# Kernel optimization log

Measured on AMD Instinct MI355X. Metric: run time of the kernel, lower is better.

## Reference

```python
import jax, jax.numpy as jnp
import numpy as np

B, L, D, H = 8, 2048, 1024, 16
FACTOR = 3


def setup_inputs() -> dict:
    key = jax.random.key(0)
    ks = jax.random.split(key, 11)
    s = 0.02
    mk = lambda k, shp: jax.random.normal(k, shp, dtype=jnp.float32)
    return {
        "queries": mk(ks[0], (B, L, D)),
        "keys": mk(ks[1], (B, L, D)),
        "values": mk(ks[2], (B, L, D)),
        "Wq": mk(ks[3], (D, D)) * s, "bq": jnp.zeros((D,), jnp.float32),
        "Wk": mk(ks[4], (D, D)) * s, "bk": jnp.zeros((D,), jnp.float32),
        "Wv": mk(ks[5], (D, D)) * s, "bv": jnp.zeros((D,), jnp.float32),
        "Wo": mk(ks[6], (D, D)) * s, "bo": jnp.zeros((D,), jnp.float32),
    }


def reference(queries, keys, values, Wq, bq, Wk, bk, Wv, bv, Wo, bo):
    b, length, d = queries.shape
    h = H
    e = d // h
    q = (queries @ Wq + bq).reshape(b, length, h, e)
    k = (keys @ Wk + bk).reshape(b, length, h, e)
    v = (values @ Wv + bv).reshape(b, length, h, e)

    # [B, H, E, L] layout for FFT along time
    qf = jnp.fft.rfft(q.transpose(0, 2, 3, 1), axis=-1)
    kf = jnp.fft.rfft(k.transpose(0, 2, 3, 1), axis=-1)
    corr = jnp.fft.irfft(qf * jnp.conj(kf), n=length, axis=-1)  # [B,H,E,L]

    vperm = v.transpose(0, 2, 3, 1)  # [B,H,E,L]
    top_k = int(FACTOR * np.log(length))  # static: 22 for L=2048
    weights, delay = jax.lax.top_k(corr, top_k)          # [B,H,E,K]
    temp_corr = jax.nn.softmax(weights, axis=-1)         # [B,H,E,K]

    idx0 = jnp.arange(length)  # [L]
    agg = jnp.zeros_like(vperm)
    # small fixed loop over top-k delays (mirrors original structure)
    for i in range(top_k):
        # faithful to source: indices wrapped mod 8 (original code quirk)
        td = (idx0[None, None, None, :] + delay[..., i:i + 1]) % 8  # [B,H,E,L]
        pattern = jnp.take_along_axis(vperm, td, axis=-1)
        agg = agg + pattern * temp_corr[..., i:i + 1]

    result = agg.transpose(0, 3, 1, 2).reshape(b, length, d)  # [B,L,D]
    out = result @ Wo + bo
    return (out, corr.transpose(0, 3, 1, 2))
```

## Files before the change

### kernel.cpp

```cpp
#include <hip/hip_runtime.h>
#include <cstdint>
#include <cstddef>


#define TOPK 22

typedef __attribute__((ext_vector_type(8))) short short8;
typedef __attribute__((ext_vector_type(4))) float f32x4;

__device__ __forceinline__ float bf2f(unsigned short u) {
  union { unsigned int i; float f; } w;
  w.i = ((unsigned int)u) << 16;
  return w.f;
}
__device__ __forceinline__ unsigned short f2bf(float f) {
  union { float f; unsigned int i; } w;
  w.f = f;
  unsigned int x = w.i;
  x += 0x7fffu + ((x >> 16) & 1u);
  return (unsigned short)(x >> 16);
}

__device__ __forceinline__ void gload_lds16(const void* g, void* l) {
  __builtin_amdgcn_global_load_lds(
      (const __attribute__((address_space(1))) unsigned int*)g,
      (__attribute__((address_space(3))) unsigned int*)l, 16, 0, 0);
}

__device__ __forceinline__ float2 make2(float x, float y) { float2 r; r.x = x; r.y = y; return r; }
__device__ __forceinline__ float2 cadd(float2 a, float2 b) { return make2(a.x + b.x, a.y + b.y); }
__device__ __forceinline__ float2 csub(float2 a, float2 b) { return make2(a.x - b.x, a.y - b.y); }
__device__ __forceinline__ float2 cmul(float2 a, float2 b) {
  return make2(a.x * b.x - a.y * b.y, a.x * b.y + a.y * b.x);
}

__device__ __forceinline__ int cfi(int u) { return 2 * u + (((u) >> 5) << 1); }

template <bool INV>
__device__ __forceinline__ void dft8(float2 (&v)[8]) {
  const float C = 0.70710678118654752f;
  float2 s0 = cadd(v[0], v[4]), s1 = csub(v[0], v[4]);
  float2 s2 = cadd(v[2], v[6]), s3 = csub(v[2], v[6]);
  float2 E0 = cadd(s0, s2), E2 = csub(s0, s2);
  float2 E1, E3;
  if (!INV) { E1 = make2(s1.x + s3.y, s1.y - s3.x); E3 = make2(s1.x - s3.y, s1.y + s3.x); }
  else      { E1 = make2(s1.x - s3.y, s1.y + s3.x); E3 = make2(s1.x + s3.y, s1.y - s3.x); }
  float2 q0 = cadd(v[1], v[5]), q1 = csub(v[1], v[5]);
  float2 q2 = cadd(v[3], v[7]), q3 = csub(v[3], v[7]);
  float2 O0 = cadd(q0, q2), O2 = csub(q0, q2);
  float2 O1, O3;
  if (!INV) { O1 = make2(q1.x + q3.y, q1.y - q3.x); O3 = make2(q1.x - q3.y, q1.y + q3.x); }
  else      { O1 = make2(q1.x - q3.y, q1.y + q3.x); O3 = make2(q1.x + q3.y, q1.y - q3.x); }
  float2 T0 = O0, T1, T2, T3;
  if (!INV) {
    T1 = make2(C * (O1.x + O1.y), C * (O1.y - O1.x));
    T2 = make2(O2.y, -O2.x);
    T3 = make2(C * (O3.y - O3.x), -C * (O3.x + O3.y));
  } else {
    T1 = make2(C * (O1.x - O1.y), C * (O1.x + O1.y));
    T2 = make2(-O2.y, O2.x);
    T3 = make2(-C * (O3.x + O3.y), C * (O3.x - O3.y));
  }
  v[0] = cadd(E0, T0); v[4] = csub(E0, T0);
  v[1] = cadd(E1, T1); v[5] = csub(E1, T1);
  v[2] = cadd(E2, T2); v[6] = csub(E2, T2);
  v[3] = cadd(E3, T3); v[7] = csub(E3, T3);
}

template <bool INV>
__device__ __forceinline__ void dft4(float2 (&v)[4]) {
  float2 s0 = cadd(v[0], v[2]), s1 = csub(v[0], v[2]);
  float2 s2 = cadd(v[1], v[3]), s3 = csub(v[1], v[3]);
  v[0] = cadd(s0, s2); v[2] = csub(s0, s2);
  if (!INV) { v[1] = make2(s1.x + s3.y, s1.y - s3.x); v[3] = make2(s1.x - s3.y, s1.y + s3.x); }
  else      { v[1] = make2(s1.x - s3.y, s1.y + s3.x); v[3] = make2(s1.x + s3.y, s1.y - s3.x); }
}

template <int NS, bool INV>
__device__ __forceinline__ void stage8(const float* __restrict__ src,
                                       float* __restrict__ dst, int tid) {
  float2 v[8];
#pragma unroll
  for (int m = 0; m < 8; ++m)
    v[m] = *reinterpret_cast<const float2*>(src + cfi(tid + (m << 8)));
  if constexpr (NS > 1) {
    const int r = tid & (NS - 1);
    const float rev = (INV ? (1.0f / (8 * NS)) : (-1.0f / (8 * NS))) * (float)r;
    float2 w1; w1.x = __builtin_amdgcn_cosf(rev); w1.y = __builtin_amdgcn_sinf(rev);
    const float2 w2 = cmul(w1, w1);
    const float2 w3 = cmul(w2, w1);
    const float2 w4 = cmul(w2, w2);
    const float2 w5 = cmul(w4, w1);
    const float2 w6 = cmul(w4, w2);
    const float2 w7 = cmul(w4, w3);
    v[1] = cmul(v[1], w1); v[2] = cmul(v[2], w2); v[3] = cmul(v[3], w3);
    v[4] = cmul(v[4], w4); v[5] = cmul(v[5], w5); v[6] = cmul(v[6], w6);
    v[7] = cmul(v[7], w7);
  }
  dft8<INV>(v);
  const int r2 = tid & (NS - 1);
  const int d = ((tid & ~(NS - 1)) << 3) | r2;
#pragma unroll
  for (int m = 0; m < 8; ++m)
    *reinterpret_cast<float2*>(dst + cfi(d + m * NS)) = v[m];
}

__device__ __forceinline__ void radix_pick(const unsigned int* h,
                                           unsigned int* sb,
                                           unsigned int need, int tid) {
  if (tid < 64) {
    const unsigned int c0 = h[4 * tid + 0];
    const unsigned int c1 = h[4 * tid + 1];
    const unsigned int c2 = h[4 * tid + 2];
    const unsigned int c3 = h[4 * tid + 3];
    const unsigned int g = c0 + c1 + c2 + c3;
    unsigned int S = g;
#pragma unroll
    for (int off = 1; off < 64; off <<= 1) {
      const unsigned int o = __shfl_down(S, off);
      if (tid + off < 64) S += o;
    }
    unsigned int A = S - g;
    int pick = -1;
    unsigned int nn = 0;
    const unsigned int cc[4] = {c0, c1, c2, c3};
#pragma unroll
    for (int j = 3; j >= 0; --j) {
      if (pick < 0) {
        if (A < need && need <= A + cc[j]) { pick = j; nn = need - A; }
        else A += cc[j];
      }
    }
    if (pick >= 0) { sb[0] = (unsigned int)(4 * tid + pick); sb[1] = nn; }
  }
}

__global__ __launch_bounds__(256) void conv_bf16(
    const float* __restrict__ q, const float* __restrict__ k,
    unsigned short* __restrict__ qb, unsigned short* __restrict__ kb) {
  const size_t nchunks = (size_t)16777216 / 8;
  for (size_t i = (size_t)blockIdx.x * 256 + threadIdx.x; i < 2 * nchunks;
       i += (size_t)gridDim.x * 256) {
    const bool isq = i < nchunks;
    const float* src = isq ? q : k;
    unsigned short* dst = isq ? qb : kb;
    const size_t c = isq ? i : i - nchunks;
    const float4 a0 = reinterpret_cast<const float4*>(src)[c * 2];
    const float4 a1 = reinterpret_cast<const float4*>(src)[c * 2 + 1];
    uint4 p;
    p.x = f2bf(a0.x) | ((unsigned int)f2bf(a0.y) << 16);
    p.y = f2bf(a0.z) | ((unsigned int)f2bf(a0.w) << 16);
    p.z = f2bf(a1.x) | ((unsigned int)f2bf(a1.y) << 16);
    p.w = f2bf(a1.z) | ((unsigned int)f2bf(a1.w) << 16);
    reinterpret_cast<uint4*>(dst)[c] = p;
  }
}

__global__ __launch_bounds__(256) void transpose_w(
    const float* __restrict__ Wq, const float* __restrict__ Wk,
    unsigned short* __restrict__ WqT, unsigned short* __restrict__ WkT) {
  __shared__ unsigned short T[64][72];
  const float* src = blockIdx.z ? Wk : Wq;
  unsigned short* dst = blockIdx.z ? WkT : WqT;
  const int k0 = blockIdx.x * 64;
  const int n0 = blockIdx.y * 64;
  const int c = threadIdx.x & 63;
  const int r0 = threadIdx.x >> 6;
#pragma unroll
  for (int p = 0; p < 16; ++p) {
    const int r = r0 + 4 * p;
    T[c][r] = f2bf(src[(size_t)(k0 + r) * 1024 + n0 + c]);
  }
  __syncthreads();
#pragma unroll
  for (int p = 0; p < 16; ++p) {
    const int nn = r0 + 4 * p;
    dst[(size_t)(n0 + nn) * 1024 + k0 + c] = T[nn][c];
  }
}

__global__ __launch_bounds__(256, 4) void gemm_qk_bf(
    const unsigned short* __restrict__ Abf,
    const unsigned short* __restrict__ WT,
    const float* __restrict__ bias,
    unsigned short* __restrict__ outT) {
  __shared__ __align__(16) unsigned short smem[16384];

  const int tid = threadIdx.x;
  const int lane = tid & 63;
  const int w = tid >> 6;
  const int wr = w >> 1, wc = w & 1;
  const int wg = blockIdx.x;
  const int sid = ((wg & 7) << 7) | (wg >> 3);
  const int m0 = (sid & 127) << 7;
  const int n0 = (sid >> 7) << 7;
  const int l15 = lane & 15;
  const int quad = lane >> 4;
  const int srow = lane >> 2;
  const int scol = (lane & 3) * 8;

  const unsigned short* Abase = Abf + (size_t)m0 * 1024;
  const unsigned short* Bbase = WT + (size_t)n0 * 1024;

  f32x4 acc[4][4];
#pragma unroll
  for (int i = 0; i < 4; ++i)
#pragma unroll
    for (int j = 0; j < 4; ++j)
#pragma unroll
      for (int r = 0; r < 4; ++r) acc[i][j][r] = 0.f;

  {
    unsigned short* As = smem;
    unsigned short* Bs = smem + 4096;
#pragma unroll
    for (int i = 0; i < 2; ++i) {
      const int cc = w * 2 + i;
      const int row = cc * 16 + srow;
      gload_lds16(Abase + (size_t)row * 1024 + scol, As + cc * 512);
      gload_lds16(Bbase + (size_t)row * 1024 + scol, Bs + cc * 512);
    }
  }
  __syncthreads();

  int cur = 0;
  for (int t = 0; t < 32; ++t) {
    if (t < 31) {
      const int k0 = (t + 1) * 32;
      unsigned short* As = smem + ((cur ^ 1) << 13);
      unsigned short* Bs = As + 4096;
#pragma unroll
      for (int i = 0; i < 2; ++i) {
        const int cc = w * 2 + i;
        const int row = cc * 16 + srow;
        gload_lds16(Abase + (size_t)row * 1024 + k0 + scol, As + cc * 512);
        gload_lds16(Bbase + (size_t)row * 1024 + k0 + scol, Bs + cc * 512);
      }
    }
    {
      const unsigned short* As = smem + (cur << 13);
      const unsigned short* Bs = As + 4096;
      short8 af[4], bfr[4];
#pragma unroll
      for (int mt = 0; mt < 4; ++mt)
        af[mt] = *reinterpret_cast<const short8*>(As + (wr * 64 + mt * 16 + l15) * 32 + quad * 8);
#pragma unroll
      for (int nt = 0; nt < 4; ++nt)
        bfr[nt] = *reinterpret_cast<const short8*>(Bs + (wc * 64 + nt * 16 + l15) * 32 + quad * 8);
#pragma unroll
      for (int mt = 0; mt < 4; ++mt)
#pragma unroll
        for (int nt = 0; nt < 4; ++nt)
          acc[mt][nt] = __builtin_amdgcn_mfma_f32_16x16x32_bf16(af[mt], bfr[nt], acc[mt][nt], 0, 0, 0);
    }
    __syncthreads();
    cur ^= 1;
  }

  unsigned short* Cs = smem;
#pragma unroll
  for (int nt = 0; nt < 4; ++nt) {
    const int n_local = wc * 64 + nt * 16 + l15;
    const float bv = bias[n0 + n_local];
#pragma unroll
    for (int mt = 0; mt < 4; ++mt) {
      const int mbase = wr * 64 + mt * 16 + quad * 4;
#pragma unroll
      for (int r = 0; r < 4; ++r)
        Cs[n_local * 128 + mbase + r] = f2bf(acc[mt][nt][r] + bv);
    }
  }
  __syncthreads();

  const int b = m0 >> 11;
  const int l0 = m0 & 2047;
  for (int it = tid; it < 2048; it += 256) {
    const int rowi = it >> 4;
    const int ci = it & 15;
    uint4 v = *reinterpret_cast<const uint4*>(Cs + rowi * 128 + ci * 8);
    *reinterpret_cast<uint4*>(outT + (size_t)(b * 1024 + n0 + rowi) * 2048 + l0 + ci * 8) = v;
  }
}

__global__ __launch_bounds__(256) void vsmall_kernel(
    const float* __restrict__ values,
    const float* __restrict__ Wv,
    const float* __restrict__ bv,
    float* __restrict__ out) {
  __shared__ float xr[1024];
  const int m = blockIdx.x;
  const int b = m >> 3, t = m & 7;
  const float* row = values + ((size_t)b * 2048 + t) * 1024;
  for (int i = threadIdx.x; i < 1024; i += 256) xr[i] = row[i];
  __syncthreads();
  const int n = blockIdx.y * 256 + threadIdx.x;
  float acc = 0.f;
#pragma unroll 8
  for (int k = 0; k < 1024; ++k) acc += xr[k] * Wv[(size_t)k * 1024 + n];
  out[(size_t)m * 1024 + n] = acc + bv[n];
}

__global__ __launch_bounds__(256, 4) void corr_topk(
    const unsigned short* __restrict__ Qt,
    const unsigned short* Kt,
    const float* __restrict__ vsmall,
    unsigned short* corrOut,
    float* __restrict__ agg) {
  __shared__ __align__(16) float bufA[4224];
  __shared__ __align__(16) float bufB[4224];

  const int tid = threadIdx.x;
  const int lane = tid & 63;
  const int wv = tid >> 6;
  const int s = blockIdx.x;
  const size_t base = (size_t)s * 2048;

  unsigned int* hist = reinterpret_cast<unsigned int*>(bufB);
  float* bins = bufB + 1024;
  float* wred = bufB + 1032;
  int* ired = reinterpret_cast<int*>(bufB + 1036);
  unsigned int* sb = reinterpret_cast<unsigned int*>(bufB + 1040);

  {
    float2 v[8];
#pragma unroll
    for (int m = 0; m < 8; ++m) {
      const int u = tid + (m << 8);
      v[m] = make2(bf2f(Qt[base + u]), bf2f(Kt[base + u]));
    }
    dft8<false>(v);
    const int d = tid << 3;
#pragma unroll
    for (int m = 0; m < 8; ++m)
      *reinterpret_cast<float2*>(bufA + cfi(d + m)) = v[m];
  }
  __syncthreads();

  stage8<8, false>(bufA, bufB, tid);
  __syncthreads();
  stage8<64, false>(bufB, bufA, tid);
  __syncthreads();

  {
#pragma unroll
    for (int h = 0; h < 2; ++h) {
      const int j = tid + (h << 8);
      float2 v[4];
#pragma unroll
      for (int m = 0; m < 4; ++m)
        v[m] = *reinterpret_cast<const float2*>(bufA + cfi(j + (m << 9)));
      const float rev = -(1.0f / 2048.0f) * (float)j;
      float2 w1; w1.x = __builtin_amdgcn_cosf(rev); w1.y = __builtin_amdgcn_sinf(rev);
      const float2 w2 = cmul(w1, w1);
      const float2 w3 = cmul(w2, w1);
      v[1] = cmul(v[1], w1); v[2] = cmul(v[2], w2); v[3] = cmul(v[3], w3);
      dft4<false>(v);
#pragma unroll
      for (int m = 0; m < 4; ++m)
        *reinterpret_cast<float2*>(bufB + cfi(j + (m << 9))) = v[m];
    }
  }
  __syncthreads();

  {
    float2 v[8];
    const float ks = 1.0f / 8192.0f;
#pragma unroll
    for (int m = 0; m < 8; ++m) {
      const int u = tid + (m << 8);
      const int ub = (2048 - u) & 2047;
      const float2 Av = *reinterpret_cast<const float2*>(bufB + cfi(u));
      const float2 Bv = *reinterpret_cast<const float2*>(bufB + cfi(ub));
      const float Px = Av.x + Bv.x, Py = Av.y - Bv.y;
      const float Qx = Av.x - Bv.x, Qy = -Av.y - Bv.y;
      const float X1 = (Px * Qx - Py * Qy) * ks;
      const float Y1 = (Px * Qy + Py * Qx) * ks;
      v[m] = make2(-Y1, X1);
    }
    dft8<true>(v);
    const int d = tid << 3;
#pragma unroll
    for (int m = 0; m < 8; ++m)
      *reinterpret_cast<float2*>(bufA + cfi(d + m)) = v[m];
  }
  __syncthreads();

  stage8<8, true>(bufA, bufB, tid);
  __syncthreads();
  stage8<64, true>(bufB, bufA, tid);
  __syncthreads();

  float cval[8];
#pragma unroll
  for (int h = 0; h < 2; ++h) {
    const int j = tid + (h << 8);
    float2 v0 = *reinterpret_cast<const float2*>(bufA + cfi(j));
    float2 v1 = *reinterpret_cast<const float2*>(bufA + cfi(j + 512));
    float2 v2 = *reinterpret_cast<const float2*>(bufA + cfi(j + 1024));
    float2 v3 = *reinterpret_cast<const float2*>(bufA + cfi(j + 1536));
    const float rev = (1.0f / 2048.0f) * (float)j;
    float2 w1; w1.x = __builtin_amdgcn_cosf(rev); w1.y = __builtin_amdgcn_sinf(rev);
    const float2 w2 = cmul(w1, w1);
    const float2 w3 = cmul(w2, w1);
    const float2 t1 = cmul(v1, w1);
    const float2 t3 = cmul(v3, w3);
    const float t2x = v2.x * w2.x - v2.y * w2.y;
    cval[h]     = v0.x + t1.x + t2x + t3.x;
    cval[h + 2] = v0.x - t1.y - t2x + t3.y;
    cval[h + 4] = v0.x - t1.x + t2x - t3.x;
    cval[h + 6] = v0.x + t1.y - t2x - t3.y;
  }

#pragma unroll
  for (int i = 0; i < 8; ++i)
    corrOut[base + (size_t)(tid + (i << 8))] = f2bf(cval[i]);

  unsigned int key[8];
#pragma unroll
  for (int i = 0; i < 8; ++i) {
    union { float f; unsigned int u; } cvt;
    cvt.f = cval[i];
    const unsigned int b = cvt.u;
    key[i] = (b & 0x80000000u) ? ~b : (b | 0x80000000u);
  }

#pragma unroll
  for (int q = 0; q < 4; ++q) hist[(q << 8) + tid] = 0u;
  if (tid < 8) bins[tid] = 0.f;
  {
    float vm = cval[0];
#pragma unroll
    for (int i = 1; i < 8; ++i) vm = fmaxf(vm, cval[i]);
#pragma unroll
    for (int off = 32; off > 0; off >>= 1) vm = fmaxf(vm, __shfl_down(vm, off));
    if (lane == 0) wred[wv] = vm;
  }
  __syncthreads();
  const float mx = fmaxf(fmaxf(wred[0], wred[1]), fmaxf(wred[2], wred[3]));

  unsigned int prefix = 0;
  unsigned int need = TOPK;
#pragma unroll
  for (int i = 0; i < 8; ++i) atomicAdd(&hist[key[i] >> 24], 1u);
  __syncthreads();
  radix_pick(hist, sb, need, tid);
  __syncthreads();
  prefix = sb[0]; need = sb[1];
#pragma unroll
  for (int i = 0; i < 8; ++i)
    if ((key[i] >> 24) == prefix) atomicAdd(&hist[256 + ((key[i] >> 16) & 255u)], 1u);
  __syncthreads();
  radix_pick(hist + 256, sb, need, tid);
  __syncthreads();
  prefix = (prefix << 8) | sb[0]; need = sb[1];
#pragma unroll
  for (int i = 0; i < 8; ++i)
    if ((key[i] >> 16) == prefix) atomicAdd(&hist[512 + ((key[i] >> 8) & 255u)], 1u);
  __syncthreads();
  radix_pick(hist + 512, sb, need, tid);
  __syncthreads();
  prefix = (prefix << 8) | sb[0]; need = sb[1];
#pragma unroll
  for (int i = 0; i < 8; ++i)
    if ((key[i] >> 8) == prefix) atomicAdd(&hist[768 + (key[i] & 255u)], 1u);
  __syncthreads();
  radix_pick(hist + 768, sb, need, tid);
  __syncthreads();
  const unsigned int T = (prefix << 8) | sb[0];
  const unsigned int takeEq = sb[1];

  unsigned int eqm = 0, selEq = 0;
#pragma unroll
  for (int i = 0; i < 8; ++i)
    if (key[i] == T) eqm |= (1u << i);
  for (unsigned int it2 = 0; it2 < takeEq; ++it2) {
    int mi = 0x7fffffff;
#pragma unroll
    for (int i = 0; i < 8; ++i)
      if (eqm & (1u << i)) mi = min(mi, tid + (i << 8));
#pragma unroll
    for (int off = 32; off > 0; off >>= 1) {
      const int o = __shfl_down(mi, off);
      if (lane + off < 64) mi = min(mi, o);
    }
    if (lane == 0) ired[wv] = mi;
    __syncthreads();
    const int gm = min(min(ired[0], ired[1]), min(ired[2], ired[3]));
#pragma unroll
    for (int i = 0; i < 8; ++i)
      if ((tid + (i << 8)) == gm) { selEq |= (1u << i); eqm &= ~(1u << i); }
    if (it2 + 1 < takeEq) __syncthreads();
  }

  float esum = 0.f;
#pragma unroll
  for (int i = 0; i < 8; ++i) {
    const bool sel = (key[i] > T) || ((selEq >> i) & 1u);
    if (sel) esum += __expf(cval[i] - mx);
  }
  if (esum > 0.f) atomicAdd(&bins[tid & 7], esum);
  __syncthreads();

  if (tid < 8) {
    const float ssum = bins[0] + bins[1] + bins[2] + bins[3] +
                       bins[4] + bins[5] + bins[6] + bins[7];
    const int b = s >> 10, n = s & 1023;
    float a = 0.f;
#pragma unroll
    for (int c = 0; c < 8; ++c)
      a += bins[c] * vsmall[(size_t)(b * 8 + ((tid + c) & 7)) * 1024 + n];
    agg[(size_t)(b * 8 + tid) * 1024 + n] = a / ssum;
  }
}

__global__ __launch_bounds__(256) void osmall_kernel(
    const float* __restrict__ aggin,
    const float* __restrict__ Wo,
    const float* __restrict__ bo,
    float* __restrict__ out) {
  __shared__ float xr[1024];
  const int m = blockIdx.x;
  const float* row = aggin + (size_t)m * 1024;
  for (int i = threadIdx.x; i < 1024; i += 256) xr[i] = row[i];
  __syncthreads();
  const int n = blockIdx.y * 256 + threadIdx.x;
  float acc = 0.f;
#pragma unroll 8
  for (int k = 0; k < 1024; ++k) acc += xr[k] * Wo[(size_t)k * 1024 + n];
  out[(size_t)m * 1024 + n] = acc + bo[n];
}

__global__ __launch_bounds__(256) void corr_transpose(
    const unsigned short* __restrict__ corrWs,
    float* __restrict__ out1) {
  __shared__ unsigned short T[64][72];
  const int bb = blockIdx.z;
  const int l0 = blockIdx.x * 64;
  const int n0 = blockIdx.y * 64;
  const int c = threadIdx.x & 63;
  const int r0 = threadIdx.x >> 6;
#pragma unroll
  for (int p = 0; p < 16; ++p) {
    const int r = r0 + 4 * p;
    T[c][r] = corrWs[(size_t)(bb * 1024 + n0 + r) * 2048 + l0 + c];
  }
  __syncthreads();
#pragma unroll
  for (int p = 0; p < 16; ++p) {
    const int ll = r0 + 4 * p;
    out1[(size_t)(bb * 2048 + l0 + ll) * 1024 + n0 + c] = bf2f(T[ll][c]);
  }
}

__global__ __launch_bounds__(256) void bcast_out(
    const float* __restrict__ outSmall,
    float* __restrict__ out0) {
  const size_t i4 = (size_t)blockIdx.x * 256 + threadIdx.x;
  const size_t basee = i4 * 4;
  const int n = (int)(basee & 1023);
  const int l = (int)((basee >> 10) & 2047);
  const int b = (int)(basee >> 21);
  const float4 v = *reinterpret_cast<const float4*>(outSmall + ((size_t)(b * 8 + (l & 7)) << 10) + n);
  *reinterpret_cast<float4*>(out0 + basee) = v;
}

extern "C" void kernel_launch(void* const* d_in, const int* in_sizes, int n_in,
                              void* d_out, int out_size, void* d_ws, size_t ws_size,
                              hipStream_t stream) {
  const float* queries = (const float*)d_in[0];
  const float* keys    = (const float*)d_in[1];
  const float* values  = (const float*)d_in[2];
  const float* Wq = (const float*)d_in[3];
  const float* bq = (const float*)d_in[4];
  const float* Wk = (const float*)d_in[5];
  const float* bk = (const float*)d_in[6];
  const float* Wv = (const float*)d_in[7];
  const float* bv = (const float*)d_in[8];
  const float* Wo = (const float*)d_in[9];
  const float* bo = (const float*)d_in[10];

  char* ws = (char*)d_ws;
  unsigned short* WqT = (unsigned short*)(ws);
  unsigned short* WkT = (unsigned short*)(ws + (2u << 20));
  unsigned short* Qt  = (unsigned short*)(ws + (4u << 20));
  float* vsmall   = (float*)(ws + (36u << 20));
  float* aggbuf   = (float*)(ws + (36u << 20) + (256u << 10));
  float* outSmall = (float*)(ws + (36u << 20) + (512u << 10));

  float* out0 = (float*)d_out;
  float* out1 = out0 + (size_t)16777216;
  unsigned short* Kt = (unsigned short*)d_out;
  unsigned short* corrWs = Kt;
  unsigned short* Qbf = (unsigned short*)out1;
  unsigned short* Kbf = Qbf + (size_t)16777216;

  conv_bf16<<<4096, 256, 0, stream>>>(queries, keys, Qbf, Kbf);
  transpose_w<<<dim3(16, 16, 2), 256, 0, stream>>>(Wq, Wk, WqT, WkT);
  gemm_qk_bf<<<1024, 256, 0, stream>>>(Qbf, WqT, bq, Qt);
  gemm_qk_bf<<<1024, 256, 0, stream>>>(Kbf, WkT, bk, Kt);
  vsmall_kernel<<<dim3(64, 4), 256, 0, stream>>>(values, Wv, bv, vsmall);
  corr_topk<<<8192, 256, 0, stream>>>(Qt, Kt, vsmall, corrWs, aggbuf);
  osmall_kernel<<<dim3(64, 4), 256, 0, stream>>>(aggbuf, Wo, bo, outSmall);
  corr_transpose<<<dim3(32, 16, 8), 256, 0, stream>>>(corrWs, out1);
  bcast_out<<<16384, 256, 0, stream>>>(outSmall, out0);
}
```

Before: 644.7 us.

## Fuse fp32-to-bf16 conversion into QK GEMM loads and fuse output projection with broadcast

Drops the standalone conversion kernel. The QK GEMM now loads fp32 activations into registers, converts them to bf16 and writes them to LDS after the MFMA step, which removes a full read-write pass over the Q and K inputs. The output projection kernel now writes its broadcast result straight into the full output, removing the intermediate buffer and one launch. In exchange, the A-operand loads in the GEMM become register-staged instead of async global_load_lds. The broadcast writes from only 256 blocks are strided, which may use less write bandwidth than the old wide broadcast kernel.

After: 655.5 us. Within noise of the previous version (+1.7%).

```diff
diff --git a/kernel.cpp b/kernel.cpp
--- a/kernel.cpp
+++ b/kernel.cpp
@@ -135,27 +135,6 @@
   }
 }
 
-__global__ __launch_bounds__(256) void conv_bf16(
-    const float* __restrict__ q, const float* __restrict__ k,
-    unsigned short* __restrict__ qb, unsigned short* __restrict__ kb) {
-  const size_t nchunks = (size_t)16777216 / 8;
-  for (size_t i = (size_t)blockIdx.x * 256 + threadIdx.x; i < 2 * nchunks;
-       i += (size_t)gridDim.x * 256) {
-    const bool isq = i < nchunks;
-    const float* src = isq ? q : k;
-    unsigned short* dst = isq ? qb : kb;
-    const size_t c = isq ? i : i - nchunks;
-    const float4 a0 = reinterpret_cast<const float4*>(src)[c * 2];
-    const float4 a1 = reinterpret_cast<const float4*>(src)[c * 2 + 1];
-    uint4 p;
-    p.x = f2bf(a0.x) | ((unsigned int)f2bf(a0.y) << 16);
-    p.y = f2bf(a0.z) | ((unsigned int)f2bf(a0.w) << 16);
-    p.z = f2bf(a1.x) | ((unsigned int)f2bf(a1.y) << 16);
-    p.w = f2bf(a1.z) | ((unsigned int)f2bf(a1.w) << 16);
-    reinterpret_cast<uint4*>(dst)[c] = p;
-  }
-}
-
 __global__ __launch_bounds__(256) void transpose_w(
     const float* __restrict__ Wq, const float* __restrict__ Wk,
     unsigned short* __restrict__ WqT, unsigned short* __restrict__ WkT) {
@@ -179,8 +158,8 @@
   }
 }
 
-__global__ __launch_bounds__(256, 4) void gemm_qk_bf(
-    const unsigned short* __restrict__ Abf,
+__global__ __launch_bounds__(256, 4) void gemm_qk(
+    const float* __restrict__ A,
     const unsigned short* __restrict__ WT,
     const float* __restrict__ bias,
     unsigned short* __restrict__ outT) {
@@ -199,7 +178,10 @@
   const int srow = lane >> 2;
   const int scol = (lane & 3) * 8;
 
-  const unsigned short* Abase = Abf + (size_t)m0 * 1024;
+  const int ar0 = tid >> 2, akc0 = (tid & 3) * 8;
+  const int ar1 = (tid + 256) >> 2, akc1 = ((tid + 256) & 3) * 8;
+  const float* Ap0 = A + (size_t)(m0 + ar0) * 1024 + akc0;
+  const float* Ap1 = A + (size_t)(m0 + ar1) * 1024 + akc1;
   const unsigned short* Bbase = WT + (size_t)n0 * 1024;
 
   f32x4 acc[4][4];
@@ -210,16 +192,32 @@
 #pragma unroll
       for (int r = 0; r < 4; ++r) acc[i][j][r] = 0.f;
 
+  float4 ra0, ra1, ra2, ra3;
+
+  ra0 = *reinterpret_cast<const float4*>(Ap0);
+  ra1 = *reinterpret_cast<const float4*>(Ap0 + 4);
+  ra2 = *reinterpret_cast<const float4*>(Ap1);
+  ra3 = *reinterpret_cast<const float4*>(Ap1 + 4);
   {
-    unsigned short* As = smem;
     unsigned short* Bs = smem + 4096;
 #pragma unroll
     for (int i = 0; i < 2; ++i) {
       const int cc = w * 2 + i;
       const int row = cc * 16 + srow;
-      gload_lds16(Abase + (size_t)row * 1024 + scol, As + cc * 512);
       gload_lds16(Bbase + (size_t)row * 1024 + scol, Bs + cc * 512);
     }
+    unsigned short* As = smem;
+    uint4 pa, pb;
+    pa.x = f2bf(ra0.x) | ((unsigned int)f2bf(ra0.y) << 16);
+    pa.y = f2bf(ra0.z) | ((unsigned int)f2bf(ra0.w) << 16);
+    pa.z = f2bf(ra1.x) | ((unsigned int)f2bf(ra1.y) << 16);
+    pa.w = f2bf(ra1.z) | ((unsigned int)f2bf(ra1.w) << 16);
+    pb.x = f2bf(ra2.x) | ((unsigned int)f2bf(ra2.y) << 16);
+    pb.y = f2bf(ra2.z) | ((unsigned int)f2bf(ra2.w) << 16);
+    pb.z = f2bf(ra3.x) | ((unsigned int)f2bf(ra3.y) << 16);
+    pb.w = f2bf(ra3.z) | ((unsigned int)f2bf(ra3.w) << 16);
+    *reinterpret_cast<uint4*>(As + ar0 * 32 + akc0) = pa;
+    *reinterpret_cast<uint4*>(As + ar1 * 32 + akc1) = pb;
   }
   __syncthreads();
 
@@ -227,13 +225,15 @@
   for (int t = 0; t < 32; ++t) {
     if (t < 31) {
       const int k0 = (t + 1) * 32;
-      unsigned short* As = smem + ((cur ^ 1) << 13);
-      unsigned short* Bs = As + 4096;
+      ra0 = *reinterpret_cast<const float4*>(Ap0 + k0);
+      ra1 = *reinterpret_cast<const float4*>(Ap0 + k0 + 4);
+      ra2 = *reinterpret_cast<const float4*>(Ap1 + k0);
+      ra3 = *reinterpret_cast<const float4*>(Ap1 + k0 + 4);
+      unsigned short* Bs = smem + ((cur ^ 1) << 13) + 4096;
 #pragma unroll
       for (int i = 0; i < 2; ++i) {
         const int cc = w * 2 + i;
         const int row = cc * 16 + srow;
-        gload_lds16(Abase + (size_t)row * 1024 + k0 + scol, As + cc * 512);
         gload_lds16(Bbase + (size_t)row * 1024 + k0 + scol, Bs + cc * 512);
       }
     }
@@ -252,6 +252,20 @@
 #pragma unroll
         for (int nt = 0; nt < 4; ++nt)
           acc[mt][nt] = __builtin_amdgcn_mfma_f32_16x16x32_bf16(af[mt], bfr[nt], acc[mt][nt], 0, 0, 0);
+    }
+    if (t < 31) {
+      unsigned short* As = smem + ((cur ^ 1) << 13);
+      uint4 pa, pb;
+      pa.x = f2bf(ra0.x) | ((unsigned int)f2bf(ra0.y) << 16);
+      pa.y = f2bf(ra0.z) | ((unsigned int)f2bf(ra0.w) << 16);
+      pa.z = f2bf(ra1.x) | ((unsigned int)f2bf(ra1.y) << 16);
+      pa.w = f2bf(ra1.z) | ((unsigned int)f2bf(ra1.w) << 16);
+      pb.x = f2bf(ra2.x) | ((unsigned int)f2bf(ra2.y) << 16);
+      pb.y = f2bf(ra2.z) | ((unsigned int)f2bf(ra2.w) << 16);
+      pb.z = f2bf(ra3.x) | ((unsigned int)f2bf(ra3.y) << 16);
+      pb.w = f2bf(ra3.z) | ((unsigned int)f2bf(ra3.w) << 16);
+      *reinterpret_cast<uint4*>(As + ar0 * 32 + akc0) = pa;
+      *reinterpret_cast<uint4*>(As + ar1 * 32 + akc1) = pb;
     }
     __syncthreads();
     cur ^= 1;
@@ -513,23 +527,6 @@
   }
 }
 
-__global__ __launch_bounds__(256) void osmall_kernel(
-    const float* __restrict__ aggin,
-    const float* __restrict__ Wo,
-    const float* __restrict__ bo,
-    float* __restrict__ out) {
-  __shared__ float xr[1024];
-  const int m = blockIdx.x;
-  const float* row = aggin + (size_t)m * 1024;
-  for (int i = threadIdx.x; i < 1024; i += 256) xr[i] = row[i];
-  __syncthreads();
-  const int n = blockIdx.y * 256 + threadIdx.x;
-  float acc = 0.f;
-#pragma unroll 8
-  for (int k = 0; k < 1024; ++k) acc += xr[k] * Wo[(size_t)k * 1024 + n];
-  out[(size_t)m * 1024 + n] = acc + bo[n];
-}
-
 __global__ __launch_bounds__(256) void corr_transpose(
     const unsigned short* __restrict__ corrWs,
     float* __restrict__ out1) {
@@ -552,16 +549,26 @@
   }
 }
 
-__global__ __launch_bounds__(256) void bcast_out(
-    const float* __restrict__ outSmall,
+__global__ __launch_bounds__(256) void osmall_bcast(
+    const float* __restrict__ aggin,
+    const float* __restrict__ Wo,
+    const float* __restrict__ bo,
     float* __restrict__ out0) {
-  const size_t i4 = (size_t)blockIdx.x * 256 + threadIdx.x;
-  const size_t basee = i4 * 4;
-  const int n = (int)(basee & 1023);
-  const int l = (int)((basee >> 10) & 2047);
-  const int b = (int)(basee >> 21);
-  const float4 v = *reinterpret_cast<const float4*>(outSmall + ((size_t)(b * 8 + (l & 7)) << 10) + n);
-  *reinterpret_cast<float4*>(out0 + basee) = v;
+  __shared__ float xr[1024];
+  const int m = blockIdx.x;
+  const int b = m >> 3, t = m & 7;
+  const float* row = aggin + (size_t)m * 1024;
+  for (int i = threadIdx.x; i < 1024; i += 256) xr[i] = row[i];
+  __syncthreads();
+  const int n = blockIdx.y * 256 + threadIdx.x;
+  float acc = 0.f;
+#pragma unroll 8
+  for (int k = 0; k < 1024; ++k) acc += xr[k] * Wo[(size_t)k * 1024 + n];
+  acc += bo[n];
+  float* o = out0 + ((size_t)b * 2048 + t) * 1024 + n;
+#pragma unroll 4
+  for (int l8 = 0; l8 < 256; ++l8)
+    o[(size_t)l8 * 8192] = acc;
 }
 
 extern "C" void kernel_launch(void* const* d_in, const int* in_sizes, int n_in,
@@ -585,22 +592,17 @@
   unsigned short* Qt  = (unsigned short*)(ws + (4u << 20));
   float* vsmall   = (float*)(ws + (36u << 20));
   float* aggbuf   = (float*)(ws + (36u << 20) + (256u << 10));
-  float* outSmall = (float*)(ws + (36u << 20) + (512u << 10));
 
   float* out0 = (float*)d_out;
   float* out1 = out0 + (size_t)16777216;
   unsigned short* Kt = (unsigned short*)d_out;
   unsigned short* corrWs = Kt;
-  unsigned short* Qbf = (unsigned short*)out1;
-  unsigned short* Kbf = Qbf + (size_t)16777216;
-
-  conv_bf16<<<4096, 256, 0, stream>>>(queries, keys, Qbf, Kbf);
+
   transpose_w<<<dim3(16, 16, 2), 256, 0, stream>>>(Wq, Wk, WqT, WkT);
-  gemm_qk_bf<<<1024, 256, 0, stream>>>(Qbf, WqT, bq, Qt);
-  gemm_qk_bf<<<1024, 256, 0, stream>>>(Kbf, WkT, bk, Kt);
+  gemm_qk<<<1024, 256, 0, stream>>>(queries, WqT, bq, Qt);
+  gemm_qk<<<1024, 256, 0, stream>>>(keys, WkT, bk, Kt);
   vsmall_kernel<<<dim3(64, 4), 256, 0, stream>>>(values, Wv, bv, vsmall);
   corr_topk<<<8192, 256, 0, stream>>>(Qt, Kt, vsmall, corrWs, aggbuf);
-  osmall_kernel<<<dim3(64, 4), 256, 0, stream>>>(aggbuf, Wo, bo, outSmall);
   corr_transpose<<<dim3(32, 16, 8), 256, 0, stream>>>(corrWs, out1);
-  bcast_out<<<16384, 256, 0, stream>>>(outSmall, out0);
-}
+  osmall_bcast<<<dim3(64, 4), 256, 0, stream>>>(aggbuf, Wo, bo, out0);
+}
```
